# Performance work log

Hardware: AMD Instinct MI355X
Metric: run time of the kernel (lower is better)

The kernel has to match this reference:

```python
import jax, jax.numpy as jnp
import numpy as np

NUM_EXPERTS = 8
TOP_K = 2
HIDDEN = 1024
INTER = 2048
BATCH, SEQ = 2, 2048


def setup_inputs() -> dict:
    key = jax.random.key(0)
    k1, k2, k3, k4 = jax.random.split(key, 4)
    hidden_states = jax.random.normal(k1, (BATCH, SEQ, HIDDEN), dtype=jnp.float32)
    # 0.02 init scale keeps router softmax unsaturated and activations sane
    router_w = jax.random.normal(k2, (NUM_EXPERTS, HIDDEN), dtype=jnp.float32) * 0.02
    up_w = jax.random.normal(k3, (NUM_EXPERTS, HIDDEN, INTER), dtype=jnp.float32) * 0.02
    down_w = jax.random.normal(k4, (NUM_EXPERTS, INTER, HIDDEN), dtype=jnp.float32) * 0.02
    return {"hidden_states": hidden_states, "router_w": router_w, "up_w": up_w, "down_w": down_w}


def reference(hidden_states, router_w, up_w, down_w):
    batch, seq_len, hidden = hidden_states.shape
    flat = hidden_states.reshape(-1, hidden)            # [N, H]
    num_tokens = flat.shape[0]

    router_logits = flat @ router_w.T                   # [N, E]
    router_probs = jax.nn.softmax(router_logits, axis=-1)
    top_weights, top_indices = jax.lax.top_k(router_probs, TOP_K)  # [N, k]
    top_weights = top_weights / jnp.sum(top_weights, axis=-1, keepdims=True)

    # scatter normalized top-k weights into a dense [N, E] mask
    rows = jnp.arange(num_tokens)[:, None]
    expert_mask = jnp.zeros((num_tokens, NUM_EXPERTS), dtype=flat.dtype)
    expert_mask = expert_mask.at[rows, top_indices].set(top_weights)

    # dense path: all experts on all tokens via batched matmul
    h = jnp.einsum('nh,ehf->enf', flat, up_w)           # [E, N, F]
    h = jax.nn.gelu(h, approximate=False)               # torch nn.GELU default = erf
    expert_out = jnp.einsum('enf,efh->enh', h, down_w)  # [E, N, H]
    output = jnp.einsum('enh,ne->nh', expert_out, expert_mask)
    output = output.reshape(batch, seq_len, hidden)

    # load-balancing aux loss; f is computed under no_grad in torch
    one_hot = jnp.zeros((num_tokens, NUM_EXPERTS), dtype=jnp.float32)
    one_hot = one_hot.at[rows, top_indices].set(1.0)
    f = jax.lax.stop_gradient(jnp.sum(one_hot, axis=0) / (num_tokens * TOP_K))
    P = jnp.mean(router_probs, axis=0)
    aux_loss = NUM_EXPERTS * jnp.sum(f * P)
    return output, aux_loss
```

## Files before the change

kernel.cpp:

```cpp
#include <hip/hip_runtime.h>
#include <math.h>

#define NE 8
#define HD 1024
#define FD 2048
#define NT 4096
#define NSLOT (NT * 2)

typedef __attribute__((ext_vector_type(8))) _Float16 half8;
typedef __attribute__((ext_vector_type(4))) float floatx4;

__device__ __forceinline__ void gload_lds(const _Float16* g, _Float16* l) {
  __builtin_amdgcn_global_load_lds(
      (const __attribute__((address_space(1))) unsigned int*)g,
      (__attribute__((address_space(3))) unsigned int*)l, 16, 0, 0);
}

__global__ void cvt_x_kernel(const float* __restrict__ x, _Float16* __restrict__ xh) {
  size_t i = (size_t)(blockIdx.x * 256 + threadIdx.x) * 8;
  float4 f0 = *(const float4*)(x + i);
  float4 f1 = *(const float4*)(x + i + 4);
  union { _Float16 h[8]; uint4 v; } u;
  u.h[0] = (_Float16)f0.x; u.h[1] = (_Float16)f0.y;
  u.h[2] = (_Float16)f0.z; u.h[3] = (_Float16)f0.w;
  u.h[4] = (_Float16)f1.x; u.h[5] = (_Float16)f1.y;
  u.h[6] = (_Float16)f1.z; u.h[7] = (_Float16)f1.w;
  *(uint4*)(xh + i) = u.v;
}

__global__ void transpose_cvt(const float* __restrict__ in, _Float16* __restrict__ outp,
                              int R, int C) {
  __shared__ float t[32][33];
  int e = blockIdx.z;
  int r0 = blockIdx.x * 32, c0 = blockIdx.y * 32;
  int tx = threadIdx.x, ty = threadIdx.y;
  const float* src = in + (size_t)e * R * C;
#pragma unroll
  for (int i = 0; i < 4; i++)
    t[ty + 8 * i][tx] = src[(size_t)(r0 + ty + 8 * i) * C + c0 + tx];
  __syncthreads();
  _Float16* dst = outp + (size_t)e * R * C;
  int tid = ty * 32 + tx;
  int cl = tid >> 3, rq = tid & 7;
  union { _Float16 h[4]; uint2 v; } o;
#pragma unroll
  for (int k = 0; k < 4; k++) o.h[k] = (_Float16)t[rq * 4 + k][cl];
  *(uint2*)(dst + (size_t)(c0 + cl) * R + r0 + rq * 4) = o.v;
}

__global__ __launch_bounds__(256) void router_probs_kernel(
    const float* __restrict__ x, const float* __restrict__ rw,
    float* __restrict__ probs, int* __restrict__ sel_e, float* __restrict__ sel_w) {
  int n = blockIdx.x * 4 + (threadIdx.x >> 6);
  int lane = threadIdx.x & 63;
  const float* xr = x + (size_t)n * HD;
  float xv[16];
#pragma unroll
  for (int t = 0; t < 16; t++) xv[t] = xr[lane + 64 * t];
  float logits[NE];
#pragma unroll
  for (int e = 0; e < NE; e++) {
    const float* w = rw + (size_t)e * HD;
    float acc = 0.f;
#pragma unroll
    for (int t = 0; t < 16; t++) acc += xv[t] * w[lane + 64 * t];
    for (int off = 32; off > 0; off >>= 1) acc += __shfl_down(acc, off);
    logits[e] = acc;
  }
  if (lane == 0) {
    float mx = logits[0];
#pragma unroll
    for (int e = 1; e < NE; e++) mx = fmaxf(mx, logits[e]);
    float p[NE]; float s = 0.f;
#pragma unroll
    for (int e = 0; e < NE; e++) { p[e] = expf(logits[e] - mx); s += p[e]; }
    float inv = 1.f / s;
#pragma unroll
    for (int e = 0; e < NE; e++) { p[e] *= inv; probs[n * NE + e] = p[e]; }
    int i1 = 0;
#pragma unroll
    for (int e = 1; e < NE; e++) if (p[e] > p[i1]) i1 = e;
    int i2 = -1; float p2 = -1.f;
#pragma unroll
    for (int e = 0; e < NE; e++) {
      if (e == i1) continue;
      if (p[e] > p2) { p2 = p[e]; i2 = e; }
    }
    float wn = 1.f / (p[i1] + p[i2]);
    sel_e[n * 2 + 0] = i1; sel_w[n * 2 + 0] = p[i1] * wn;
    sel_e[n * 2 + 1] = i2; sel_w[n * 2 + 1] = p[i2] * wn;
  }
}

__global__ __launch_bounds__(1024) void router_reduce_kernel(
    const float* __restrict__ probs, const int* __restrict__ sel_e,
    int* __restrict__ counts, int* __restrict__ offs, int* __restrict__ cursor,
    float* __restrict__ aux_out) {
  int t = threadIdx.x;
  int lane = t & 63, wave = t >> 6;
  float ps[NE];
  int cn[NE];
#pragma unroll
  for (int e = 0; e < NE; e++) { ps[e] = 0.f; cn[e] = 0; }
  for (int r = t; r < NT; r += 1024) {
    const float* pr = probs + (size_t)r * NE;
#pragma unroll
    for (int e = 0; e < NE; e++) ps[e] += pr[e];
  }
  for (int i = t; i < NSLOT; i += 1024) {
    int e = sel_e[i];
#pragma unroll
    for (int j = 0; j < NE; j++) cn[j] += (e == j) ? 1 : 0;
  }
  for (int off = 32; off > 0; off >>= 1) {
#pragma unroll
    for (int e = 0; e < NE; e++) {
      ps[e] += __shfl_down(ps[e], off);
      cn[e] += __shfl_down(cn[e], off);
    }
  }
  __shared__ float sps[16][NE];
  __shared__ int scn[16][NE];
  if (lane == 0) {
#pragma unroll
    for (int e = 0; e < NE; e++) { sps[wave][e] = ps[e]; scn[wave][e] = cn[e]; }
  }
  __syncthreads();
  if (t == 0) {
    float tot_p[NE]; int tot_c[NE];
#pragma unroll
    for (int e = 0; e < NE; e++) { tot_p[e] = 0.f; tot_c[e] = 0; }
    for (int w = 0; w < 16; w++)
#pragma unroll
      for (int e = 0; e < NE; e++) { tot_p[e] += sps[w][e]; tot_c[e] += scn[w][e]; }
    int o = 0;
    float aux = 0.f;
    for (int e = 0; e < NE; e++) {
      counts[e] = tot_c[e];
      offs[e] = o; o += tot_c[e];
      cursor[e] = 0;
      aux += ((float)tot_c[e] / (float)NSLOT) * (tot_p[e] / (float)NT);
    }
    aux_out[0] = (float)NE * aux;
  }
}

__global__ __launch_bounds__(256) void build_gather(
    const int* __restrict__ sel_e, const float* __restrict__ sel_w,
    const int* __restrict__ offs, int* __restrict__ cursor,
    int* __restrict__ gtok, float* __restrict__ gw, int* __restrict__ srow) {
  __shared__ int lh[NE], lbase[NE];
  int t = threadIdx.x;
  int i = blockIdx.x * 256 + t;
  if (t < NE) lh[t] = 0;
  __syncthreads();
  int e = sel_e[i];
  int lrank = atomicAdd(&lh[e], 1);
  __syncthreads();
  if (t < NE) lbase[t] = atomicAdd(&cursor[t], lh[t]);
  __syncthreads();
  int row = offs[e] + lbase[e] + lrank;
  gtok[row] = i >> 1;
  gw[row] = sel_w[i];
  srow[i] = row;
}

template <int KDIM, int NDIM, bool IS_UP>
__global__ __launch_bounds__(256, 3) void moe_gemm2(
    const _Float16* __restrict__ Abase, const _Float16* __restrict__ Bt,
    const int* __restrict__ counts, const int* __restrict__ offs,
    const int* __restrict__ gtok, const float* __restrict__ gw,
    _Float16* __restrict__ Hout, float* __restrict__ Dout) {
  int e = blockIdx.x;
  int cnt = counts[e];
  int m0 = blockIdx.y * 128;
  if (m0 >= cnt) return;
  int n0 = blockIdx.z * 128;
  int off = offs[e];

  __shared__ __align__(16) _Float16 As[128 * 64];
  __shared__ __align__(16) _Float16 Bs[128 * 64];

  int tid = threadIdx.x;
  int lane = tid & 63, wave = tid >> 6;
  int wm = (wave >> 1) * 64, wn = (wave & 1) * 64;

  int srow8 = lane >> 3;
  int chunk = (lane & 7) ^ srow8;
  const _Float16* ga[4];
  const _Float16* gb[4];
  _Float16* lA[4];
  _Float16* lB[4];
#pragma unroll
  for (int j = 0; j < 4; j++) {
    int r = wave * 32 + j * 8 + srow8;
    int am = m0 + r;
    if (am > cnt - 1) am = cnt - 1;
    if (IS_UP) {
      ga[j] = Abase + (size_t)gtok[off + am] * KDIM + chunk * 8;
    } else {
      ga[j] = Abase + (size_t)(off + am) * KDIM + chunk * 8;
    }
    gb[j] = Bt + ((size_t)e * NDIM + n0 + r) * KDIM + chunk * 8;
    lA[j] = As + (wave * 32 + j * 8) * 64;
    lB[j] = Bs + (wave * 32 + j * 8) * 64;
  }

  floatx4 acc[4][4];
#pragma unroll
  for (int i = 0; i < 4; i++)
#pragma unroll
    for (int j = 0; j < 4; j++) acc[i][j] = (floatx4){0.f, 0.f, 0.f, 0.f};

  int fr = lane & 15, g = lane >> 4;
  int sw0 = ((g) ^ (fr & 7)) * 8;
  int sw1 = ((4 + g) ^ (fr & 7)) * 8;

  for (int kt = 0; kt < KDIM / 64; kt++) {
    __syncthreads();
#pragma unroll
    for (int j = 0; j < 4; j++) gload_lds(ga[j], lA[j]);
#pragma unroll
    for (int j = 0; j < 4; j++) gload_lds(gb[j], lB[j]);
#pragma unroll
    for (int j = 0; j < 4; j++) { ga[j] += 64; gb[j] += 64; }
    __syncthreads();

    half8 af[4], bfv[4];
#pragma unroll
    for (int t = 0; t < 4; t++) {
      af[t] = *(const half8*)(As + (wm + t * 16 + fr) * 64 + sw0);
      bfv[t] = *(const half8*)(Bs + (wn + t * 16 + fr) * 64 + sw0);
    }
#pragma unroll
    for (int i = 0; i < 4; i++)
#pragma unroll
      for (int j = 0; j < 4; j++)
        acc[i][j] = __builtin_amdgcn_mfma_f32_16x16x32_f16(af[i], bfv[j], acc[i][j], 0, 0, 0);
#pragma unroll
    for (int t = 0; t < 4; t++) {
      af[t] = *(const half8*)(As + (wm + t * 16 + fr) * 64 + sw1);
      bfv[t] = *(const half8*)(Bs + (wn + t * 16 + fr) * 64 + sw1);
    }
#pragma unroll
    for (int i = 0; i < 4; i++)
#pragma unroll
      for (int j = 0; j < 4; j++)
        acc[i][j] = __builtin_amdgcn_mfma_f32_16x16x32_f16(af[i], bfv[j], acc[i][j], 0, 0, 0);
  }

  int cq = (lane >> 4) * 4, cc = lane & 15;
#pragma unroll
  for (int i = 0; i < 4; i++) {
#pragma unroll
    for (int r = 0; r < 4; r++) {
      int m = wm + i * 16 + cq + r;
      if (m0 + m < cnt) {
        if (IS_UP) {
          float w = gw[off + m0 + m];
          _Float16* hrow = Hout + (size_t)(off + m0 + m) * NDIM + n0;
#pragma unroll
          for (int j = 0; j < 4; j++) {
            float v = acc[i][j][r];
            float gl = 0.5f * v * (1.f + erff(v * 0.70710678118f));
            hrow[wn + j * 16 + cc] = (_Float16)(gl * w);
          }
        } else {
          float* orow = Dout + (size_t)(off + m0 + m) * NDIM + n0;
#pragma unroll
          for (int j = 0; j < 4; j++) orow[wn + j * 16 + cc] = acc[i][j][r];
        }
      }
    }
  }
}

__global__ __launch_bounds__(256) void combine_kernel(
    const float* __restrict__ Dout, const int* __restrict__ srow,
    float* __restrict__ out) {
  int n = blockIdx.x;
  int t = threadIdx.x;
  int r0 = srow[n * 2], r1 = srow[n * 2 + 1];
  float4 a = *(const float4*)(Dout + (size_t)r0 * HD + t * 4);
  float4 b = *(const float4*)(Dout + (size_t)r1 * HD + t * 4);
  float4 c; c.x = a.x + b.x; c.y = a.y + b.y; c.z = a.z + b.z; c.w = a.w + b.w;
  *(float4*)(out + (size_t)n * HD + t * 4) = c;
}

extern "C" void kernel_launch(void* const* d_in, const int* in_sizes, int n_in,
                              void* d_out, int out_size, void* d_ws, size_t ws_size,
                              hipStream_t stream) {
  const float* x = (const float*)d_in[0];
  const float* rw = (const float*)d_in[1];
  const float* up_w = (const float*)d_in[2];
  const float* dn_w = (const float*)d_in[3];
  float* out = (float*)d_out;

  char* ws = (char*)d_ws;
  _Float16* Xh   = (_Float16*)(ws + 0);
  _Float16* Wut  = (_Float16*)(ws + 8388608);
  float*    Dout = (float*)(ws + 0);
  _Float16* Wdt  = (_Float16*)(ws + 41943040);
  _Float16* Hbuf = (_Float16*)(ws + 75497472);
  char* tail = ws + 109051904;
  int*   gtok   = (int*)(tail + 0);
  float* gw     = (float*)(tail + 32768);
  int*   sel_e  = (int*)(tail + 65536);
  float* sel_w  = (float*)(tail + 98304);
  int*   srow   = (int*)(tail + 131072);
  float* probs  = (float*)(tail + 163840);
  int*   counts = (int*)(tail + 294912);
  int*   offs   = (int*)(tail + 294944);
  int*   cursor = (int*)(tail + 294976);

  cvt_x_kernel<<<(NT * HD / 8) / 256, 256, 0, stream>>>(x, Xh);
  transpose_cvt<<<dim3(HD / 32, FD / 32, NE), dim3(32, 8), 0, stream>>>(up_w, Wut, HD, FD);
  transpose_cvt<<<dim3(FD / 32, HD / 32, NE), dim3(32, 8), 0, stream>>>(dn_w, Wdt, FD, HD);
  router_probs_kernel<<<NT / 4, 256, 0, stream>>>(x, rw, probs, sel_e, sel_w);
  router_reduce_kernel<<<1, 1024, 0, stream>>>(probs, sel_e, counts, offs, cursor,
                                               out + (size_t)NT * HD);
  build_gather<<<NSLOT / 256, 256, 0, stream>>>(sel_e, sel_w, offs, cursor, gtok, gw, srow);

  moe_gemm2<HD, FD, true><<<dim3(NE, 32, FD / 128), 256, 0, stream>>>(
      Xh, Wut, counts, offs, gtok, gw, Hbuf, nullptr);
  moe_gemm2<FD, HD, false><<<dim3(NE, 32, HD / 128), 256, 0, stream>>>(
      Hbuf, Wdt, counts, offs, gtok, gw, nullptr, Dout);
  combine_kernel<<<NT, 256, 0, stream>>>(Dout, srow, out);
}
```

Measured before the change: 316.9 us.

## Double-buffer up GEMM, fp16 down output, vectorized transpose loads

Splits the templated grouped GEMM into separate up and down kernels. The up GEMM gets a double-buffered LDS pipeline, so the next K-tile's global-to-LDS load overlaps the MFMAs on the current tile, at the cost of dropping occupancy to 2 blocks per CU. The down GEMM now writes fp16 instead of fp32, halving intermediate traffic into the combine kernel at some precision cost. The weight transpose now loads with float4 on a 1D 256-thread block.

```diff
diff --git a/kernel.cpp b/kernel.cpp
--- a/kernel.cpp
+++ b/kernel.cpp
@@ -8,6 +8,7 @@
 #define NSLOT (NT * 2)
 
 typedef __attribute__((ext_vector_type(8))) _Float16 half8;
+typedef __attribute__((ext_vector_type(4))) _Float16 half4f;
 typedef __attribute__((ext_vector_type(4))) float floatx4;
 
 __device__ __forceinline__ void gload_lds(const _Float16* g, _Float16* l) {
@@ -33,14 +34,15 @@
   __shared__ float t[32][33];
   int e = blockIdx.z;
   int r0 = blockIdx.x * 32, c0 = blockIdx.y * 32;
-  int tx = threadIdx.x, ty = threadIdx.y;
+  int tid = threadIdx.x;
   const float* src = in + (size_t)e * R * C;
-#pragma unroll
-  for (int i = 0; i < 4; i++)
-    t[ty + 8 * i][tx] = src[(size_t)(r0 + ty + 8 * i) * C + c0 + tx];
+  {
+    int row = tid >> 3, c4 = (tid & 7) * 4;
+    float4 v = *(const float4*)(src + (size_t)(r0 + row) * C + c0 + c4);
+    t[row][c4] = v.x; t[row][c4 + 1] = v.y; t[row][c4 + 2] = v.z; t[row][c4 + 3] = v.w;
+  }
   __syncthreads();
   _Float16* dst = outp + (size_t)e * R * C;
-  int tid = ty * 32 + tx;
   int cl = tid >> 3, rq = tid & 7;
   union { _Float16 h[4]; uint2 v; } o;
 #pragma unroll
@@ -165,12 +167,12 @@
   srow[i] = row;
 }
 
-template <int KDIM, int NDIM, bool IS_UP>
-__global__ __launch_bounds__(256, 3) void moe_gemm2(
+__global__ __launch_bounds__(256, 2) void moe_gemm_up(
     const _Float16* __restrict__ Abase, const _Float16* __restrict__ Bt,
     const int* __restrict__ counts, const int* __restrict__ offs,
     const int* __restrict__ gtok, const float* __restrict__ gw,
-    _Float16* __restrict__ Hout, float* __restrict__ Dout) {
+    _Float16* __restrict__ Hout) {
+  constexpr int KDIM = HD, NDIM = FD, TK = KDIM / 64;
   int e = blockIdx.x;
   int cnt = counts[e];
   int m0 = blockIdx.y * 128;
@@ -178,6 +180,107 @@
   int n0 = blockIdx.z * 128;
   int off = offs[e];
 
+  __shared__ __align__(16) _Float16 sm[2 * 16384];
+
+  int tid = threadIdx.x;
+  int lane = tid & 63, wave = tid >> 6;
+  int wm = (wave >> 1) * 64, wn = (wave & 1) * 64;
+
+  int srow8 = lane >> 3;
+  int chunk = (lane & 7) ^ srow8;
+  const _Float16* ga[4];
+  const _Float16* gb[4];
+  int lAo[4], lBo[4];
+#pragma unroll
+  for (int j = 0; j < 4; j++) {
+    int r = wave * 32 + j * 8 + srow8;
+    int am = m0 + r;
+    if (am > cnt - 1) am = cnt - 1;
+    ga[j] = Abase + (size_t)gtok[off + am] * KDIM + chunk * 8;
+    gb[j] = Bt + ((size_t)e * NDIM + n0 + r) * KDIM + chunk * 8;
+    lAo[j] = (wave * 32 + j * 8) * 64;
+    lBo[j] = 8192 + lAo[j];
+  }
+
+  floatx4 acc[4][4];
+#pragma unroll
+  for (int i = 0; i < 4; i++)
+#pragma unroll
+    for (int j = 0; j < 4; j++) acc[i][j] = (floatx4){0.f, 0.f, 0.f, 0.f};
+
+  int fr = lane & 15, g = lane >> 4;
+  int sw0 = ((g) ^ (fr & 7)) * 8;
+  int sw1 = ((4 + g) ^ (fr & 7)) * 8;
+
+  auto issue = [&](int b) {
+    _Float16* base = sm + b * 16384;
+#pragma unroll
+    for (int j = 0; j < 4; j++) { gload_lds(ga[j], base + lAo[j]); ga[j] += 64; }
+#pragma unroll
+    for (int j = 0; j < 4; j++) { gload_lds(gb[j], base + lBo[j]); gb[j] += 64; }
+  };
+  issue(0);
+
+  for (int kt = 0; kt < TK; kt++) {
+    __syncthreads();
+    if (kt + 1 < TK) issue((kt + 1) & 1);
+    const _Float16* As = sm + (kt & 1) * 16384;
+    const _Float16* Bs = As + 8192;
+    half8 af[4], bfv[4];
+#pragma unroll
+    for (int t = 0; t < 4; t++) {
+      af[t] = *(const half8*)(As + (wm + t * 16 + fr) * 64 + sw0);
+      bfv[t] = *(const half8*)(Bs + (wn + t * 16 + fr) * 64 + sw0);
+    }
+#pragma unroll
+    for (int i = 0; i < 4; i++)
+#pragma unroll
+      for (int j = 0; j < 4; j++)
+        acc[i][j] = __builtin_amdgcn_mfma_f32_16x16x32_f16(af[i], bfv[j], acc[i][j], 0, 0, 0);
+#pragma unroll
+    for (int t = 0; t < 4; t++) {
+      af[t] = *(const half8*)(As + (wm + t * 16 + fr) * 64 + sw1);
+      bfv[t] = *(const half8*)(Bs + (wn + t * 16 + fr) * 64 + sw1);
+    }
+#pragma unroll
+    for (int i = 0; i < 4; i++)
+#pragma unroll
+      for (int j = 0; j < 4; j++)
+        acc[i][j] = __builtin_amdgcn_mfma_f32_16x16x32_f16(af[i], bfv[j], acc[i][j], 0, 0, 0);
+  }
+
+  int cq = (lane >> 4) * 4, cc = lane & 15;
+#pragma unroll
+  for (int i = 0; i < 4; i++) {
+#pragma unroll
+    for (int r = 0; r < 4; r++) {
+      int m = wm + i * 16 + cq + r;
+      if (m0 + m < cnt) {
+        float w = gw[off + m0 + m];
+        _Float16* hrow = Hout + (size_t)(off + m0 + m) * NDIM + n0;
+#pragma unroll
+        for (int j = 0; j < 4; j++) {
+          float v = acc[i][j][r];
+          float gl = 0.5f * v * (1.f + erff(v * 0.70710678118f));
+          hrow[wn + j * 16 + cc] = (_Float16)(gl * w);
+        }
+      }
+    }
+  }
+}
+
+__global__ __launch_bounds__(256, 3) void moe_gemm_dn(
+    const _Float16* __restrict__ Abase, const _Float16* __restrict__ Bt,
+    const int* __restrict__ counts, const int* __restrict__ offs,
+    _Float16* __restrict__ Dout) {
+  constexpr int KDIM = FD, NDIM = HD;
+  int e = blockIdx.x;
+  int cnt = counts[e];
+  int m0 = blockIdx.y * 128;
+  if (m0 >= cnt) return;
+  int n0 = blockIdx.z * 128;
+  int off = offs[e];
+
   __shared__ __align__(16) _Float16 As[128 * 64];
   __shared__ __align__(16) _Float16 Bs[128 * 64];
 
@@ -196,11 +299,7 @@
     int r = wave * 32 + j * 8 + srow8;
     int am = m0 + r;
     if (am > cnt - 1) am = cnt - 1;
-    if (IS_UP) {
-      ga[j] = Abase + (size_t)gtok[off + am] * KDIM + chunk * 8;
-    } else {
-      ga[j] = Abase + (size_t)(off + am) * KDIM + chunk * 8;
-    }
+    ga[j] = Abase + (size_t)(off + am) * KDIM + chunk * 8;
     gb[j] = Bt + ((size_t)e * NDIM + n0 + r) * KDIM + chunk * 8;
     lA[j] = As + (wave * 32 + j * 8) * 64;
     lB[j] = Bs + (wave * 32 + j * 8) * 64;
@@ -256,34 +355,27 @@
     for (int r = 0; r < 4; r++) {
       int m = wm + i * 16 + cq + r;
       if (m0 + m < cnt) {
-        if (IS_UP) {
-          float w = gw[off + m0 + m];
-          _Float16* hrow = Hout + (size_t)(off + m0 + m) * NDIM + n0;
-#pragma unroll
-          for (int j = 0; j < 4; j++) {
-            float v = acc[i][j][r];
-            float gl = 0.5f * v * (1.f + erff(v * 0.70710678118f));
-            hrow[wn + j * 16 + cc] = (_Float16)(gl * w);
-          }
-        } else {
-          float* orow = Dout + (size_t)(off + m0 + m) * NDIM + n0;
-#pragma unroll
-          for (int j = 0; j < 4; j++) orow[wn + j * 16 + cc] = acc[i][j][r];
-        }
+        _Float16* orow = Dout + (size_t)(off + m0 + m) * NDIM + n0;
+#pragma unroll
+        for (int j = 0; j < 4; j++) orow[wn + j * 16 + cc] = (_Float16)acc[i][j][r];
       }
     }
   }
 }
 
 __global__ __launch_bounds__(256) void combine_kernel(
-    const float* __restrict__ Dout, const int* __restrict__ srow,
+    const _Float16* __restrict__ D, const int* __restrict__ srow,
     float* __restrict__ out) {
   int n = blockIdx.x;
   int t = threadIdx.x;
   int r0 = srow[n * 2], r1 = srow[n * 2 + 1];
-  float4 a = *(const float4*)(Dout + (size_t)r0 * HD + t * 4);
-  float4 b = *(const float4*)(Dout + (size_t)r1 * HD + t * 4);
-  float4 c; c.x = a.x + b.x; c.y = a.y + b.y; c.z = a.z + b.z; c.w = a.w + b.w;
+  half4f a = *(const half4f*)(D + (size_t)r0 * HD + t * 4);
+  half4f b = *(const half4f*)(D + (size_t)r1 * HD + t * 4);
+  float4 c;
+  c.x = (float)a[0] + (float)b[0];
+  c.y = (float)a[1] + (float)b[1];
+  c.z = (float)a[2] + (float)b[2];
+  c.w = (float)a[3] + (float)b[3];
   *(float4*)(out + (size_t)n * HD + t * 4) = c;
 }
 
@@ -299,7 +391,7 @@
   char* ws = (char*)d_ws;
   _Float16* Xh   = (_Float16*)(ws + 0);
   _Float16* Wut  = (_Float16*)(ws + 8388608);
-  float*    Dout = (float*)(ws + 0);
+  _Float16* Dh   = (_Float16*)(ws + 0);
   _Float16* Wdt  = (_Float16*)(ws + 41943040);
   _Float16* Hbuf = (_Float16*)(ws + 75497472);
   char* tail = ws + 109051904;
@@ -314,16 +406,16 @@
   int*   cursor = (int*)(tail + 294976);
 
   cvt_x_kernel<<<(NT * HD / 8) / 256, 256, 0, stream>>>(x, Xh);
-  transpose_cvt<<<dim3(HD / 32, FD / 32, NE), dim3(32, 8), 0, stream>>>(up_w, Wut, HD, FD);
-  transpose_cvt<<<dim3(FD / 32, HD / 32, NE), dim3(32, 8), 0, stream>>>(dn_w, Wdt, FD, HD);
+  transpose_cvt<<<dim3(HD / 32, FD / 32, NE), 256, 0, stream>>>(up_w, Wut, HD, FD);
+  transpose_cvt<<<dim3(FD / 32, HD / 32, NE), 256, 0, stream>>>(dn_w, Wdt, FD, HD);
   router_probs_kernel<<<NT / 4, 256, 0, stream>>>(x, rw, probs, sel_e, sel_w);
   router_reduce_kernel<<<1, 1024, 0, stream>>>(probs, sel_e, counts, offs, cursor,
                                                out + (size_t)NT * HD);
   build_gather<<<NSLOT / 256, 256, 0, stream>>>(sel_e, sel_w, offs, cursor, gtok, gw, srow);
 
-  moe_gemm2<HD, FD, true><<<dim3(NE, 32, FD / 128), 256, 0, stream>>>(
-      Xh, Wut, counts, offs, gtok, gw, Hbuf, nullptr);
-  moe_gemm2<FD, HD, false><<<dim3(NE, 32, HD / 128), 256, 0, stream>>>(
-      Hbuf, Wdt, counts, offs, gtok, gw, nullptr, Dout);
-  combine_kernel<<<NT, 256, 0, stream>>>(Dout, srow, out);
-}
+  moe_gemm_up<<<dim3(NE, 32, FD / 128), 256, 0, stream>>>(
+      Xh, Wut, counts, offs, gtok, gw, Hbuf);
+  moe_gemm_dn<<<dim3(NE, 32, HD / 128), 256, 0, stream>>>(
+      Hbuf, Wdt, counts, offs, Dh);
+  combine_kernel<<<NT, 256, 0, stream>>>(Dh, srow, out);
+}
```

Measured after the change: 320.4 us. Within noise of the previous version (+1.1%).
